# Kernel tuning notes

Measured on AMD Instinct MI355X. Metric: run time of the kernel, lower is better.

The kernel has to match this reference:

```python
import jax, jax.numpy as jnp
import numpy as np

WIN = 7          # window_size (square)
N = WIN * WIN    # tokens per window = 49
C = 384          # channels
H = 12           # heads
HD = C // H      # head dim = 32
NW = 4           # shifted-window mask groups
BW = 4096        # total windows (batch*num_windows)
SCALE = HD ** -0.5


def _relative_position_index():
    coords_h = np.arange(WIN)
    coords_w = np.arange(WIN)
    coords = np.stack(np.meshgrid(coords_h, coords_w, indexing='ij'))  # [2,7,7]
    cf = coords.reshape(2, -1)                                         # [2,49]
    rel = cf[:, :, None] - cf[:, None, :]                              # [2,49,49]
    rel = rel.transpose(1, 2, 0)
    rel[:, :, 0] += WIN - 1
    rel[:, :, 1] += WIN - 1
    rel[:, :, 0] *= 2 * WIN - 1
    return rel.sum(-1).astype(np.int32)                                # [49,49]


def setup_inputs() -> dict:
    key = jax.random.key(0)
    ks = jax.random.split(key, 7)
    x = jax.random.normal(ks[0], (BW, N, C), dtype=jnp.float32)
    mask = jax.random.normal(ks[1], (NW, N, N), dtype=jnp.float32)
    w_qkv = jax.random.normal(ks[2], (C, 3 * C), dtype=jnp.float32) * 0.02
    b_qkv = jnp.zeros((3 * C,), dtype=jnp.float32)
    bias_table = jax.random.normal(ks[3], ((2 * WIN - 1) ** 2, H), dtype=jnp.float32) * 0.02
    w_proj = jax.random.normal(ks[4], (C, C), dtype=jnp.float32) * 0.02
    b_proj = jnp.zeros((C,), dtype=jnp.float32)
    rel_index = jnp.asarray(_relative_position_index())
    return {"x": x, "mask": mask, "w_qkv": w_qkv, "b_qkv": b_qkv,
            "bias_table": bias_table, "w_proj": w_proj, "b_proj": b_proj,
            "rel_index": rel_index}


def reference(x, mask, w_qkv, b_qkv, bias_table, w_proj, b_proj, rel_index):
    B = x.shape[0]
    # QKV projection: [B,N,3C] -> [3,B,H,N,hd]
    qkv = x @ w_qkv + b_qkv
    qkv = qkv.reshape(B, N, 3, H, HD).transpose(2, 0, 3, 1, 4)
    q, k, v = qkv[0], qkv[1], qkv[2]
    q = q * SCALE
    attn = jnp.einsum('bhnd,bhmd->bhnm', q, k)          # [B,H,N,N]
    # gathered relative position bias: [N,N,H] -> [H,N,N]
    bias = bias_table[rel_index]                         # [N,N,H]
    attn = attn + bias.transpose(2, 0, 1)[None]
    # shift-window mask add
    attn = attn.reshape(B // NW, NW, H, N, N) + mask[None, :, None]
    attn = attn.reshape(B, H, N, N)
    attn = jax.nn.softmax(attn, axis=-1)
    out = jnp.einsum('bhnm,bhmd->bhnd', attn, v)         # [B,H,N,hd]
    out = out.transpose(0, 2, 1, 3).reshape(B, N, C)
    out = out @ w_proj + b_proj
    return out
```

## Files before the change

kernel.cpp:

```cpp
#include <hip/hip_runtime.h>

typedef unsigned short u16;
typedef u16 u16x4 __attribute__((ext_vector_type(4)));
typedef u16 u16x8 __attribute__((ext_vector_type(8)));
typedef __bf16 bf16x8 __attribute__((ext_vector_type(8)));
typedef float f32x4 __attribute__((ext_vector_type(4)));

#define MFMA16 __builtin_amdgcn_mfma_f32_16x16x32_bf16
#define QSCALE 0.17677669529663689f
#define VMWAIT(N) asm volatile("s_waitcnt vmcnt(" #N ")" ::: "memory")

__device__ __forceinline__ u16 f2bf(float f) {
  unsigned u = __builtin_bit_cast(unsigned, f);
  u += 0x7fffu + ((u >> 16) & 1u);
  return (u16)(u >> 16);
}
__device__ __forceinline__ bf16x8 as_bf(u16x8 u) { return __builtin_bit_cast(bf16x8, u); }
__device__ __forceinline__ f32x4 zf4() { f32x4 z = {0.f, 0.f, 0.f, 0.f}; return z; }

template <int CTRL>
__device__ __forceinline__ float dppf(float x) {
  int i = __builtin_bit_cast(int, x);
  int r = __builtin_amdgcn_update_dpp(i, i, CTRL, 0xf, 0xf, false);
  return __builtin_bit_cast(float, r);
}
__device__ __forceinline__ float rmax16(float x) {
  x = fmaxf(x, dppf<0xB1>(x));
  x = fmaxf(x, dppf<0x4E>(x));
  x = fmaxf(x, dppf<0x124>(x));
  x = fmaxf(x, dppf<0x128>(x));
  return x;
}
__device__ __forceinline__ float rsum16(float x) {
  x += dppf<0xB1>(x);
  x += dppf<0x4E>(x);
  x += dppf<0x124>(x);
  x += dppf<0x128>(x);
  return x;
}

__global__ __launch_bounds__(256) void prep_kernel(
    const float* __restrict__ wq, const float* __restrict__ wp,
    const float* __restrict__ bt, const int* __restrict__ ri,
    const float* __restrict__ mask,
    u16* __restrict__ wqT, u16* __restrict__ wpT, float* __restrict__ smask2) {
  int idx = blockIdx.x * 256 + threadIdx.x;
  if (idx < 442368) {
    int nn = idx / 384, kk = idx % 384;
    wqT[idx] = f2bf(wq[(size_t)kk * 1152 + nn]);
  } else if (idx < 589824) {
    int i2 = idx - 442368;
    int nn = i2 / 384, kk = i2 % 384;
    wpT[i2] = f2bf(wp[(size_t)kk * 384 + nn]);
  } else if (idx < 740352) {
    int i3 = idx - 589824;
    int g = i3 / 37632;
    int rem = i3 % 37632;
    int h = rem / 3136;
    int nm = rem % 3136;
    int n = nm >> 6;
    int r2 = nm & 63;
    int lane = r2 >> 2, nj = r2 & 3;
    int m = nj * 16 + lane;
    float v = 0.f;
    if (m < 49 && n < 49)
      v = bt[ri[n * 49 + m] * 12 + h] + mask[g * 2401 + n * 49 + m];
    smask2[i3] = v;
  }
}

__global__ __launch_bounds__(256) void conv_x(const float* __restrict__ x,
                                              u16* __restrict__ xb) {
  size_t i = ((size_t)blockIdx.x * 256 + threadIdx.x) * 8;
  f32x4 a = *(const f32x4*)(x + i);
  f32x4 b = *(const f32x4*)(x + i + 4);
  u16x8 o;
  o[0] = f2bf(a[0]); o[1] = f2bf(a[1]); o[2] = f2bf(a[2]); o[3] = f2bf(a[3]);
  o[4] = f2bf(b[0]); o[5] = f2bf(b[1]); o[6] = f2bf(b[2]); o[7] = f2bf(b[3]);
  *(u16x8*)(xb + i) = o;
}

template <int NCH, bool QKV>
__global__ __launch_bounds__(256) void gemm4(
    const u16* __restrict__ Wt, const u16* __restrict__ Xb,
    const float* __restrict__ bias, void* __restrict__ outp) {
  __shared__ u16 As[2][128 * 32];
  __shared__ u16 Bs[2][128 * 32];
  const int t = threadIdx.x;
  const int l = t & 63, w = t >> 6;

  const int bid = blockIdx.x;
  const int xcd = bid & 7, q = bid >> 3;
  const int logical = xcd * (196 * NCH) + q;
  const int tokt = logical / NCH, cht = logical % NCH;
  const int tb = tokt * 128;
  const int cb = cht * 128;
  const int LDC = NCH * 128;

  f32x4 acc[4][4];
#pragma unroll
  for (int mi = 0; mi < 4; ++mi)
#pragma unroll
    for (int ni = 0; ni < 4; ++ni) acc[mi][ni] = zf4();

  const int rA = (w >> 1) * 64 + (l & 15);
  const int rB = (w & 1) * 64 + (l & 15);
  const int gsel = l >> 4;
  const int gA = ((gsel ^ ((rA >> 1) & 3))) * 8;
  const int gB = ((gsel ^ ((rB >> 1) & 3))) * 8;

  auto stage = [&](int bf, int kt) {
    const int ko = kt * 32;
#pragma unroll
    for (int j = 0; j < 2; ++j) {
      const int gi = j * 256 + t;
      const int row = gi >> 2, slot = gi & 3;
      const int sg = (slot ^ ((row >> 1) & 3)) * 8;
      __builtin_amdgcn_global_load_lds(
          (const __attribute__((address_space(1))) unsigned int*)
              (Wt + (size_t)(cb + row) * 384 + ko + sg),
          (__attribute__((address_space(3))) unsigned int*)(&As[bf][gi * 8]),
          16, 0, 0);
      __builtin_amdgcn_global_load_lds(
          (const __attribute__((address_space(1))) unsigned int*)
              (Xb + (size_t)(tb + row) * 384 + ko + sg),
          (__attribute__((address_space(3))) unsigned int*)(&Bs[bf][gi * 8]),
          16, 0, 0);
    }
  };

  auto kbody = [&](int cur, int ktnext, bool dostage) {
    __builtin_amdgcn_sched_barrier(0);
    __builtin_amdgcn_s_barrier();
    bf16x8 af[4], bfr[4];
#pragma unroll
    for (int mi = 0; mi < 4; ++mi)
      af[mi] = *(const bf16x8*)(&As[cur][(rA + mi * 16) * 32 + gA]);
#pragma unroll
    for (int nj = 0; nj < 4; ++nj)
      bfr[nj] = *(const bf16x8*)(&Bs[cur][(rB + nj * 16) * 32 + gB]);
    asm volatile("s_waitcnt lgkmcnt(0)" ::: "memory");
    __builtin_amdgcn_sched_barrier(0);
    __builtin_amdgcn_s_barrier();
    if (dostage) stage(cur, ktnext);
    __builtin_amdgcn_sched_barrier(0);
    __builtin_amdgcn_s_setprio(1);
#pragma unroll
    for (int mi = 0; mi < 4; ++mi)
#pragma unroll
      for (int nj = 0; nj < 4; ++nj)
        acc[mi][nj] = MFMA16(af[mi], bfr[nj], acc[mi][nj], 0, 0, 0);
    __builtin_amdgcn_s_setprio(0);
  };

  stage(0, 0);
  stage(1, 1);
#pragma unroll
  for (int kt = 0; kt < 10; ++kt) {
    VMWAIT(4);
    kbody(kt & 1, kt + 2, true);
  }
  VMWAIT(4);
  kbody(0, 0, false);
  VMWAIT(0);
  kbody(1, 0, false);

#pragma unroll
  for (int mi = 0; mi < 4; ++mi) {
    const int ch = cb + (w >> 1) * 64 + mi * 16 + (l >> 4) * 4;
    const f32x4 bv = *(const f32x4*)(bias + ch);
#pragma unroll
    for (int nj = 0; nj < 4; ++nj) {
      const int tok = tb + (w & 1) * 64 + nj * 16 + (l & 15);
      if constexpr (QKV) {
        const int qkvi = ch / 384;
        const int rem = ch - qkvi * 384;
        const int hh = rem >> 5;
        const int d = rem & 31;
        const float scl = (qkvi == 0) ? QSCALE : 1.0f;
        u16x4 pk;
#pragma unroll
        for (int r = 0; r < 4; ++r) pk[r] = f2bf((acc[mi][nj][r] + bv[r]) * scl);
        *(u16x4*)((u16*)outp + ((size_t)(qkvi * 12 + hh) * 200704 + tok) * 32 + d) = pk;
      } else {
        f32x4 o;
#pragma unroll
        for (int r = 0; r < 4; ++r) o[r] = acc[mi][nj][r] + bv[r];
        *(f32x4*)((float*)outp + (size_t)tok * LDC + ch) = o;
      }
    }
  }
}

__global__ __launch_bounds__(256) void attn_kernel(
    const u16* __restrict__ qkvb, const float* __restrict__ smask2,
    u16* __restrict__ attnb) {
  __shared__ u16 Pl[4][4096];
  __shared__ u16 Vt[4][2336];
  const int t = threadIdx.x;
  const int l = t & 63, wv = t >> 6;
  const int bid = blockIdx.x;
  const int logical = (bid & 7) * 1536 + (bid >> 3);
  const int b = logical / 3;
  const int hg = logical % 3;
  const int h = hg * 4 + wv;
  u16* Pw = &Pl[wv][0];
  u16* Vw = &Vt[wv][0];
  const u16x8 z = {0, 0, 0, 0, 0, 0, 0, 0};

#pragma unroll
  for (int i = 0; i < 4; ++i) {
    const int row = i * 16 + (l >> 2);
    const int sg = l & 3;
    u16x8 vv = z;
    if (row < 49)
      vv = *(const u16x8*)(qkvb + ((size_t)(24 + h) * 200704 + b * 49 + row) * 32 + sg * 8);
#pragma unroll
    for (int e = 0; e < 8; ++e) {
      const int d = sg * 8 + e;
      Vw[d * 72 + (d >> 3) * 8 + row] = vv[e];
    }
  }

  const u16* qb = qkvb + ((size_t)h * 200704 + b * 49) * 32 + (l >> 4) * 8;
  const u16* kp = qkvb + ((size_t)(12 + h) * 200704 + b * 49) * 32 + (l >> 4) * 8;
  bf16x8 qa[4], kb[4];
#pragma unroll
  for (int mi = 0; mi < 4; ++mi) {
    const int n = mi * 16 + (l & 15);
    qa[mi] = (n < 49) ? *(const bf16x8*)(qb + n * 32) : as_bf(z);
    kb[mi] = (n < 49) ? *(const bf16x8*)(kp + n * 32) : as_bf(z);
  }

  f32x4 s[4][4];
  __builtin_amdgcn_s_setprio(1);
#pragma unroll
  for (int mi = 0; mi < 4; ++mi)
#pragma unroll
    for (int nj = 0; nj < 4; ++nj) s[mi][nj] = MFMA16(qa[mi], kb[nj], zf4(), 0, 0, 0);
  __builtin_amdgcn_s_setprio(0);

  const float* sm2 = smask2 + ((size_t)(b & 3) * 12 + h) * 3136;
#pragma unroll
  for (int mi = 0; mi < 4; ++mi) {
#pragma unroll
    for (int r = 0; r < 4; ++r) {
      const int n = mi * 16 + (l >> 4) * 4 + r;
      if (n < 49) {
        const f32x4 bv = *(const f32x4*)(sm2 + n * 64 + (l & 15) * 4);
        s[mi][0][r] += bv[0];
        s[mi][1][r] += bv[1];
        s[mi][2][r] += bv[2];
        s[mi][3][r] = ((l & 15) == 0) ? s[mi][3][r] + bv[3] : -1e30f;
      }
    }
  }
#pragma unroll
  for (int mi = 0; mi < 4; ++mi) {
#pragma unroll
    for (int r = 0; r < 4; ++r) {
      float mx = fmaxf(fmaxf(s[mi][0][r], s[mi][1][r]), fmaxf(s[mi][2][r], s[mi][3][r]));
      mx = rmax16(mx);
      float e0 = 0.f;
#pragma unroll
      for (int nj = 0; nj < 4; ++nj) {
        const float p = __expf(s[mi][nj][r] - mx);
        s[mi][nj][r] = p;
        e0 += p;
      }
      e0 = rsum16(e0);
      const float inv = 1.0f / e0;
#pragma unroll
      for (int nj = 0; nj < 4; ++nj) s[mi][nj][r] *= inv;
    }
  }
#pragma unroll
  for (int mi = 0; mi < 4; ++mi)
#pragma unroll
    for (int r = 0; r < 4; ++r) {
      const int row = mi * 16 + (l >> 4) * 4 + r;
#pragma unroll
      for (int nj = 0; nj < 4; ++nj) {
        const int col = nj * 16 + (l & 15);
        Pw[row * 64 + (((col >> 3) ^ (row & 7)) * 8) + (col & 7)] = f2bf(s[mi][nj][r]);
      }
    }
  asm volatile("s_waitcnt lgkmcnt(0)" ::: "memory");
  __builtin_amdgcn_sched_barrier(0);

  f32x4 ot[2][4];
#pragma unroll
  for (int dj = 0; dj < 2; ++dj)
#pragma unroll
    for (int mi = 0; mi < 4; ++mi) ot[dj][mi] = zf4();
#pragma unroll
  for (int ks = 0; ks < 2; ++ks) {
    bf16x8 va[2], pb[4];
#pragma unroll
    for (int dj = 0; dj < 2; ++dj) {
      const int d0 = dj * 16 + (l & 15);
      va[dj] = *(const bf16x8*)(Vw + d0 * 72 + (d0 >> 3) * 8 + ks * 32 + (l >> 4) * 8);
    }
#pragma unroll
    for (int mi = 0; mi < 4; ++mi) {
      const int row = mi * 16 + (l & 15);
      pb[mi] = *(const bf16x8*)(Pw + row * 64 + (((ks * 4 + (l >> 4)) ^ (l & 7)) * 8));
    }
    __builtin_amdgcn_s_setprio(1);
#pragma unroll
    for (int dj = 0; dj < 2; ++dj)
#pragma unroll
      for (int mi = 0; mi < 4; ++mi)
        ot[dj][mi] = MFMA16(va[dj], pb[mi], ot[dj][mi], 0, 0, 0);
    __builtin_amdgcn_s_setprio(0);
  }
#pragma unroll
  for (int dj = 0; dj < 2; ++dj)
#pragma unroll
    for (int mi = 0; mi < 4; ++mi) {
      const int n = mi * 16 + (l & 15);
      if (n < 49) {
        u16x4 pk;
        pk[0] = f2bf(ot[dj][mi][0]);
        pk[1] = f2bf(ot[dj][mi][1]);
        pk[2] = f2bf(ot[dj][mi][2]);
        pk[3] = f2bf(ot[dj][mi][3]);
        *(u16x4*)(attnb + (size_t)(b * 49 + n) * 384 + h * 32 + dj * 16 + (l >> 4) * 4) = pk;
      }
    }
}

extern "C" void kernel_launch(void* const* d_in, const int* in_sizes, int n_in,
                              void* d_out, int out_size, void* d_ws, size_t ws_size,
                              hipStream_t stream) {
  const float* x       = (const float*)d_in[0];
  const float* mask    = (const float*)d_in[1];
  const float* w_qkv   = (const float*)d_in[2];
  const float* b_qkv   = (const float*)d_in[3];
  const float* bias_t  = (const float*)d_in[4];
  const float* w_proj  = (const float*)d_in[5];
  const float* b_proj  = (const float*)d_in[6];
  const int*   rel_idx = (const int*)d_in[7];
  float* out = (float*)d_out;

  char* ws = (char*)d_ws;
  u16*   wqT    = (u16*)ws;
  u16*   wpT    = (u16*)(ws + 884736);
  float* smask2 = (float*)(ws + 1179648);
  u16*   qkvb   = (u16*)(ws + 1781760);
  u16*   xb     = (u16*)(ws + 464203776);
  u16*   attnb  = (u16*)(ws + 464203776);

  prep_kernel<<<2892, 256, 0, stream>>>(w_qkv, w_proj, bias_t, rel_idx, mask,
                                        wqT, wpT, smask2);
  conv_x<<<37632, 256, 0, stream>>>(x, xb);
  gemm4<9, true><<<14112, 256, 0, stream>>>(wqT, xb, b_qkv, qkvb);
  attn_kernel<<<12288, 256, 0, stream>>>(qkvb, smask2, attnb);
  gemm4<3, false><<<4704, 256, 0, stream>>>(wpT, attnb, b_proj, out);
}
```

Baseline: 740.5 us.

## Fuse fp32-to-bf16 conversion of x into the QKV GEMM tile loads

Removes the separate conv_x pass and has the QKV GEMM stream fp32 x tiles directly into LDS with an XOR swizzle, converting to bf16 when fragments are read. This drops a full write and re-read of the bf16 copy of x (about 150MB of fp32 input). In exchange the QKV kernel loads twice the bytes per B tile, uses more LDS, issues more global_load_lds ops per stage, and repeats the conversion across the 9 channel tiles that share each token tile.

```diff
diff --git a/kernel.cpp b/kernel.cpp
--- a/kernel.cpp
+++ b/kernel.cpp
@@ -69,21 +69,128 @@
   }
 }
 
-__global__ __launch_bounds__(256) void conv_x(const float* __restrict__ x,
-                                              u16* __restrict__ xb) {
-  size_t i = ((size_t)blockIdx.x * 256 + threadIdx.x) * 8;
-  f32x4 a = *(const f32x4*)(x + i);
-  f32x4 b = *(const f32x4*)(x + i + 4);
-  u16x8 o;
-  o[0] = f2bf(a[0]); o[1] = f2bf(a[1]); o[2] = f2bf(a[2]); o[3] = f2bf(a[3]);
-  o[4] = f2bf(b[0]); o[5] = f2bf(b[1]); o[6] = f2bf(b[2]); o[7] = f2bf(b[3]);
-  *(u16x8*)(xb + i) = o;
-}
-
-template <int NCH, bool QKV>
-__global__ __launch_bounds__(256) void gemm4(
+__global__ __launch_bounds__(256) void gemm_qkv(
+    const u16* __restrict__ Wt, const float* __restrict__ X,
+    const float* __restrict__ bias, u16* __restrict__ outp) {
+  __shared__ u16 As[2][128 * 32];
+  __shared__ float Bs[2][128 * 32];
+  const int t = threadIdx.x;
+  const int l = t & 63, w = t >> 6;
+
+  const int bid = blockIdx.x;
+  const int xcd = bid & 7, q = bid >> 3;
+  const int logical = xcd * (196 * 9) + q;
+  const int tokt = logical / 9, cht = logical % 9;
+  const int tb = tokt * 128;
+  const int cb = cht * 128;
+
+  f32x4 acc[4][4];
+#pragma unroll
+  for (int mi = 0; mi < 4; ++mi)
+#pragma unroll
+    for (int ni = 0; ni < 4; ++ni) acc[mi][ni] = zf4();
+
+  const int rA = (w >> 1) * 64 + (l & 15);
+  const int rB = (w & 1) * 64 + (l & 15);
+  const int gsel = l >> 4;
+  const int gA = ((gsel ^ ((rA >> 1) & 3))) * 8;
+  const int mB = rB & 7;
+
+  auto stage = [&](int bf, int kt) {
+    const int ko = kt * 32;
+#pragma unroll
+    for (int j = 0; j < 2; ++j) {
+      const int gi = j * 256 + t;
+      const int row = gi >> 2, slot = gi & 3;
+      const int sg = (slot ^ ((row >> 1) & 3)) * 8;
+      __builtin_amdgcn_global_load_lds(
+          (const __attribute__((address_space(1))) unsigned int*)
+              (Wt + (size_t)(cb + row) * 384 + ko + sg),
+          (__attribute__((address_space(3))) unsigned int*)(&As[bf][gi * 8]),
+          16, 0, 0);
+    }
+#pragma unroll
+    for (int j = 0; j < 4; ++j) {
+      const int gi = j * 256 + t;
+      const int row = gi >> 3, slot = gi & 7;
+      const int sg = (slot ^ (row & 7)) * 4;
+      __builtin_amdgcn_global_load_lds(
+          (const __attribute__((address_space(1))) unsigned int*)
+              (X + (size_t)(tb + row) * 384 + ko + sg),
+          (__attribute__((address_space(3))) unsigned int*)(&Bs[bf][gi * 4]),
+          16, 0, 0);
+    }
+  };
+
+  auto kbody = [&](int cur, int ktnext, bool dostage) {
+    __builtin_amdgcn_sched_barrier(0);
+    __builtin_amdgcn_s_barrier();
+    bf16x8 af[4], bfr[4];
+#pragma unroll
+    for (int mi = 0; mi < 4; ++mi)
+      af[mi] = *(const bf16x8*)(&As[cur][(rA + mi * 16) * 32 + gA]);
+#pragma unroll
+    for (int nj = 0; nj < 4; ++nj) {
+      const int row = rB + nj * 16;
+      const float* bp = &Bs[cur][row * 32];
+      const f32x4 lo = *(const f32x4*)(bp + (((gsel * 2) ^ mB) * 4));
+      const f32x4 hi = *(const f32x4*)(bp + (((gsel * 2 + 1) ^ mB) * 4));
+      bf16x8 r;
+      r[0] = (__bf16)lo[0]; r[1] = (__bf16)lo[1];
+      r[2] = (__bf16)lo[2]; r[3] = (__bf16)lo[3];
+      r[4] = (__bf16)hi[0]; r[5] = (__bf16)hi[1];
+      r[6] = (__bf16)hi[2]; r[7] = (__bf16)hi[3];
+      bfr[nj] = r;
+    }
+    asm volatile("s_waitcnt lgkmcnt(0)" ::: "memory");
+    __builtin_amdgcn_sched_barrier(0);
+    __builtin_amdgcn_s_barrier();
+    if (dostage) stage(cur, ktnext);
+    __builtin_amdgcn_sched_barrier(0);
+    __builtin_amdgcn_s_setprio(1);
+#pragma unroll
+    for (int mi = 0; mi < 4; ++mi)
+#pragma unroll
+      for (int nj = 0; nj < 4; ++nj)
+        acc[mi][nj] = MFMA16(af[mi], bfr[nj], acc[mi][nj], 0, 0, 0);
+    __builtin_amdgcn_s_setprio(0);
+  };
+
+  stage(0, 0);
+  stage(1, 1);
+#pragma unroll
+  for (int kt = 0; kt < 10; ++kt) {
+    VMWAIT(6);
+    kbody(kt & 1, kt + 2, true);
+  }
+  VMWAIT(6);
+  kbody(0, 0, false);
+  VMWAIT(0);
+  kbody(1, 0, false);
+
+#pragma unroll
+  for (int mi = 0; mi < 4; ++mi) {
+    const int ch = cb + (w >> 1) * 64 + mi * 16 + (l >> 4) * 4;
+    const f32x4 bv = *(const f32x4*)(bias + ch);
+    const int qkvi = ch / 384;
+    const int rem = ch - qkvi * 384;
+    const int hh = rem >> 5;
+    const int d = rem & 31;
+    const float scl = (qkvi == 0) ? QSCALE : 1.0f;
+#pragma unroll
+    for (int nj = 0; nj < 4; ++nj) {
+      const int tok = tb + (w & 1) * 64 + nj * 16 + (l & 15);
+      u16x4 pk;
+#pragma unroll
+      for (int r = 0; r < 4; ++r) pk[r] = f2bf((acc[mi][nj][r] + bv[r]) * scl);
+      *(u16x4*)(outp + ((size_t)(qkvi * 12 + hh) * 200704 + tok) * 32 + d) = pk;
+    }
+  }
+}
+
+__global__ __launch_bounds__(256) void gemm_proj(
     const u16* __restrict__ Wt, const u16* __restrict__ Xb,
-    const float* __restrict__ bias, void* __restrict__ outp) {
+    const float* __restrict__ bias, float* __restrict__ outp) {
   __shared__ u16 As[2][128 * 32];
   __shared__ u16 Bs[2][128 * 32];
   const int t = threadIdx.x;
@@ -91,11 +198,10 @@
 
   const int bid = blockIdx.x;
   const int xcd = bid & 7, q = bid >> 3;
-  const int logical = xcd * (196 * NCH) + q;
-  const int tokt = logical / NCH, cht = logical % NCH;
+  const int logical = xcd * (196 * 3) + q;
+  const int tokt = logical / 3, cht = logical % 3;
   const int tb = tokt * 128;
   const int cb = cht * 128;
-  const int LDC = NCH * 128;
 
   f32x4 acc[4][4];
 #pragma unroll
@@ -172,22 +278,10 @@
 #pragma unroll
     for (int nj = 0; nj < 4; ++nj) {
       const int tok = tb + (w & 1) * 64 + nj * 16 + (l & 15);
-      if constexpr (QKV) {
-        const int qkvi = ch / 384;
-        const int rem = ch - qkvi * 384;
-        const int hh = rem >> 5;
-        const int d = rem & 31;
-        const float scl = (qkvi == 0) ? QSCALE : 1.0f;
-        u16x4 pk;
-#pragma unroll
-        for (int r = 0; r < 4; ++r) pk[r] = f2bf((acc[mi][nj][r] + bv[r]) * scl);
-        *(u16x4*)((u16*)outp + ((size_t)(qkvi * 12 + hh) * 200704 + tok) * 32 + d) = pk;
-      } else {
-        f32x4 o;
-#pragma unroll
-        for (int r = 0; r < 4; ++r) o[r] = acc[mi][nj][r] + bv[r];
-        *(f32x4*)((float*)outp + (size_t)tok * LDC + ch) = o;
-      }
+      f32x4 o;
+#pragma unroll
+      for (int r = 0; r < 4; ++r) o[r] = acc[mi][nj][r] + bv[r];
+      *(f32x4*)(outp + (size_t)tok * 384 + ch) = o;
     }
   }
 }
@@ -348,13 +442,11 @@
   u16*   wpT    = (u16*)(ws + 884736);
   float* smask2 = (float*)(ws + 1179648);
   u16*   qkvb   = (u16*)(ws + 1781760);
-  u16*   xb     = (u16*)(ws + 464203776);
   u16*   attnb  = (u16*)(ws + 464203776);
 
   prep_kernel<<<2892, 256, 0, stream>>>(w_qkv, w_proj, bias_t, rel_idx, mask,
                                         wqT, wpT, smask2);
-  conv_x<<<37632, 256, 0, stream>>>(x, xb);
-  gemm4<9, true><<<14112, 256, 0, stream>>>(wqT, xb, b_qkv, qkvb);
+  gemm_qkv<<<14112, 256, 0, stream>>>(wqT, x, b_qkv, qkvb);
   attn_kernel<<<12288, 256, 0, stream>>>(qkvb, smask2, attnb);
-  gemm4<3, false><<<4704, 256, 0, stream>>>(wpT, attnb, b_proj, out);
-}
+  gemm_proj<<<4704, 256, 0, stream>>>(wpT, attnb, b_proj, out);
+}
```

Measured after the change: 791.4 us. +6.9%, slower.
